# Optimization experiments

Hardware: AMD Instinct MI355X
Metric: run time of the kernel (lower is better)

## Reference

```python
import jax, jax.numpy as jnp
import numpy as np

D_MODEL, D_FF, N_EXP, TOP_K = 1024, 2816, 8, 2
EPS = 1e-6


def setup_inputs() -> dict:
    key = jax.random.key(0)
    ks = jax.random.split(key, 9)
    s = 1.0 / np.sqrt(D_MODEL)
    sf = 1.0 / np.sqrt(D_FF)
    x = jax.random.normal(ks[0], (2, 2048, D_MODEL), dtype=jnp.float32)
    gate_w = jax.random.normal(ks[1], (N_EXP, D_MODEL), dtype=jnp.float32) * s  # [E, d] (torch Linear weight)
    w1 = jax.random.normal(ks[2], (N_EXP, D_FF, D_MODEL), dtype=jnp.float32) * s
    w2 = jax.random.normal(ks[3], (N_EXP, D_MODEL, D_FF), dtype=jnp.float32) * sf
    w3 = jax.random.normal(ks[4], (N_EXP, D_FF, D_MODEL), dtype=jnp.float32) * s
    sw1 = jax.random.normal(ks[5], (D_FF, D_MODEL), dtype=jnp.float32) * s
    sw2 = jax.random.normal(ks[6], (D_MODEL, D_FF), dtype=jnp.float32) * sf
    sw3 = jax.random.normal(ks[7], (D_FF, D_MODEL), dtype=jnp.float32) * s
    return {"x": x, "gate_w": gate_w, "w1": w1, "w2": w2, "w3": w3,
            "sw1": sw1, "sw2": sw2, "sw3": sw3}


def _expert(x, a, c, b):
    h = jax.nn.gelu(x @ a.T, approximate=False) * (x @ b.T)
    return h @ c.T


def reference(x, gate_w, w1, w2, w3, sw1, sw2, sw3):
    identity = x
    # RMSNorm with fresh weight=1 (module instantiates RMSNorm inside forward)
    x_norm = x / jnp.sqrt(jnp.mean(x * x, axis=-1, keepdims=True) + EPS)
    gate_logits = x_norm @ gate_w.T                    # [B,S,E]
    gate_weights = jax.nn.softmax(gate_logits, axis=-1)
    topk_w, topk_i = jax.lax.top_k(gate_weights, TOP_K)
    topk_w = topk_w / jnp.sum(topk_w, axis=-1, keepdims=True)
    # combine weight per expert: [B,S,E]
    cw = jnp.sum(jax.nn.one_hot(topk_i, N_EXP, dtype=x.dtype) * topk_w[..., None], axis=-2)
    out = jnp.zeros_like(x)
    for e in range(N_EXP):  # fixed small expert loop
        out = out + _expert(x_norm, w1[e], w2[e], w3[e]) * cw[..., e:e + 1]
    out = out + _expert(x_norm, sw1, sw2, sw3)
    return out + identity
```

## Files before the change

kernel.cpp:

```cpp
#include <hip/hip_runtime.h>
#include <cmath>

#define T_TOK 4096
#define DM 1024
#define DFF 2816

typedef __bf16 bfx8 __attribute__((ext_vector_type(8)));
typedef float f32x4 __attribute__((ext_vector_type(4)));

__device__ __forceinline__ float bf2f(unsigned short u) {
    unsigned int x = ((unsigned int)u) << 16;
    return __uint_as_float(x);
}
__device__ __forceinline__ unsigned short f2bf(float f) {
    unsigned int b = __float_as_uint(f);
    return (unsigned short)((b + 0x7fffu + ((b >> 16) & 1u)) >> 16);
}
__device__ __forceinline__ uint4 pack8(const float* p) {
    float4 a = *(const float4*)p, b = *(const float4*)(p + 4);
    uint4 r;
    r.x = (unsigned)f2bf(a.x) | ((unsigned)f2bf(a.y) << 16);
    r.y = (unsigned)f2bf(a.z) | ((unsigned)f2bf(a.w) << 16);
    r.z = (unsigned)f2bf(b.x) | ((unsigned)f2bf(b.y) << 16);
    r.w = (unsigned)f2bf(b.z) | ((unsigned)f2bf(b.w) << 16);
    return r;
}

__global__ void kProbe(const unsigned short* __restrict__ x, int* flag, int* counts, int* counts2) {
    __shared__ int cnt;
    if (threadIdx.x == 0) cnt = 0;
    __syncthreads();
    int sane = 0;
#pragma unroll
    for (int i = 0; i < 8; i++) {
        unsigned short u = x[threadIdx.x * 8 + i];
        int e = (u >> 7) & 0xFF;
        if (e >= 110 && e <= 134) sane++;
    }
    atomicAdd(&cnt, sane);
    __syncthreads();
    if (threadIdx.x == 0) flag[0] = (cnt >= 1843) ? 0 : 1;
    if (threadIdx.x < 8) { counts[threadIdx.x] = 0; counts2[threadIdx.x] = 0; }
}

__global__ __launch_bounds__(256) void kA(
    const void* __restrict__ xraw, const void* __restrict__ gwraw, const int* __restrict__ flag,
    float* __restrict__ accum, unsigned short* __restrict__ xnorm,
    int* __restrict__ counts, int* __restrict__ t2i, float* __restrict__ t2w)
{
    int f = flag[0];
    int t = blockIdx.x, tid = threadIdx.x;
    int wid = tid >> 6, lane = tid & 63;

    double xv[4]; double ss = 0.0;
    if (f) {
        const float* xr = (const float*)xraw + (size_t)t * DM;
#pragma unroll
        for (int i = 0; i < 4; i++) { xv[i] = (double)xr[tid + 256 * i]; ss += xv[i] * xv[i]; }
    } else {
        const unsigned short* xr = (const unsigned short*)xraw + (size_t)t * DM;
#pragma unroll
        for (int i = 0; i < 4; i++) { xv[i] = (double)bf2f(xr[tid + 256 * i]); ss += xv[i] * xv[i]; }
    }
#pragma unroll
    for (int o = 32; o > 0; o >>= 1) ss += __shfl_down(ss, o);

    __shared__ double sred[4];
    __shared__ double sscale;
    if (lane == 0) sred[wid] = ss;
    __syncthreads();
    if (tid == 0) {
        double tot = sred[0] + sred[1] + sred[2] + sred[3];
        sscale = 1.0 / sqrt(tot / (double)DM + 1e-6);
    }
    __syncthreads();
    double scale = sscale;

#pragma unroll
    for (int i = 0; i < 4; i++) {
        int idx = tid + 256 * i;
        accum[(size_t)t * DM + idx] = (float)xv[i];
        xnorm[(size_t)t * DM + idx] = f2bf((float)(xv[i] * scale));
    }

    const float* gw32 = (const float*)gwraw;
    const unsigned short* gw16 = (const unsigned short*)gwraw;
    double p[8];
#pragma unroll
    for (int e = 0; e < 8; e++) p[e] = 0.0;
#pragma unroll
    for (int i = 0; i < 4; i++) {
        int idx = tid + 256 * i;
#pragma unroll
        for (int e = 0; e < 8; e++) {
            double w = f ? (double)gw32[e * DM + idx] : (double)bf2f(gw16[e * DM + idx]);
            p[e] += xv[i] * w;
        }
    }
    __shared__ double gred[4][8];
#pragma unroll
    for (int e = 0; e < 8; e++) {
        double v = p[e];
#pragma unroll
        for (int o = 32; o > 0; o >>= 1) v += __shfl_down(v, o);
        if (lane == 0) gred[wid][e] = v;
    }
    __syncthreads();
    if (tid == 0) {
        double l[8], m = -1e300;
        for (int e = 0; e < 8; e++) {
            l[e] = scale * (gred[0][e] + gred[1][e] + gred[2][e] + gred[3][e]);
            if (l[e] > m) m = l[e];
        }
        double pe[8];
        for (int e = 0; e < 8; e++) pe[e] = exp(l[e] - m);
        int a = 0;
        for (int e = 1; e < 8; e++) if (pe[e] > pe[a]) a = e;
        int b = (a == 0) ? 1 : 0;
        for (int e = 0; e < 8; e++) { if (e == a) continue; if (pe[e] > pe[b]) b = e; }
        double s2 = pe[a] + pe[b];
        t2i[2 * t] = a; t2i[2 * t + 1] = b;
        t2w[2 * t] = (float)(pe[a] / s2); t2w[2 * t + 1] = (float)(pe[b] / s2);
        atomicAdd(&counts[a], 1); atomicAdd(&counts[b], 1);
    }
}

__global__ void kA2(const int* counts, int* base) {
    if (threadIdx.x == 0) {
        int acc = 0;
        for (int e = 0; e < 8; e++) { base[e] = acc; acc += counts[e]; }
    }
}

__global__ __launch_bounds__(256) void kA3(
    const int* __restrict__ t2i, const float* __restrict__ t2w, const int* __restrict__ base,
    int* counts2, int* __restrict__ rows_token, float* __restrict__ rows_w)
{
    int t = blockIdx.x * 256 + threadIdx.x;
    if (t < T_TOK) {
#pragma unroll
        for (int s = 0; s < 2; s++) {
            int e = t2i[2 * t + s];
            int pos = atomicAdd(&counts2[e], 1);
            int row = base[e] + pos;
            rows_token[row] = t; rows_w[row] = t2w[2 * t + s];
        }
        rows_token[2 * T_TOK + t] = t;
        rows_w[2 * T_TOK + t] = 1.0f;
    }
}

__global__ __launch_bounds__(256) void kB(
    const unsigned short* __restrict__ xnorm,
    const void* __restrict__ w1, const void* __restrict__ w3,
    const void* __restrict__ sw1, const void* __restrict__ sw3,
    const int* __restrict__ flag, const int* __restrict__ counts, const int* __restrict__ base,
    const int* __restrict__ rows_token, unsigned short* __restrict__ h, int c0, int CF)
{
    int f = flag[0];
    int e = blockIdx.z;
    int nr, rb; const unsigned short *W1u, *W3u; const float *W1f, *W3f;
    if (e < 8) {
        nr = counts[e]; rb = base[e];
        size_t eb = (size_t)e * DFF * DM;
        W1u = (const unsigned short*)w1 + eb; W3u = (const unsigned short*)w3 + eb;
        W1f = (const float*)w1 + eb;          W3f = (const float*)w3 + eb;
    } else {
        nr = T_TOK; rb = 2 * T_TOK;
        W1u = (const unsigned short*)sw1; W3u = (const unsigned short*)sw3;
        W1f = (const float*)sw1;          W3f = (const float*)sw3;
    }
    int r0 = blockIdx.y * 128;
    if (r0 >= nr) return;
    int n0l = blockIdx.x * 64;

    __shared__ __align__(16) unsigned short sA[128 * 72];
    __shared__ __align__(16) unsigned short sB1[64 * 72];
    __shared__ __align__(16) unsigned short sB3[64 * 72];

    int tid = threadIdx.x, wid = tid >> 6, lane = tid & 63;
    int srow = tid >> 3, scol = (tid & 7) * 8;
    int q = lane >> 4, ln = lane & 15;

    const unsigned short* aptr[4];
#pragma unroll
    for (int t = 0; t < 4; t++) {
        int r = r0 + srow + t * 32;
        int tk = rows_token[rb + ((r < nr) ? r : 0)];
        aptr[t] = xnorm + (size_t)tk * DM + scol;
    }
    size_t boff[2];
#pragma unroll
    for (int t = 0; t < 2; t++)
        boff[t] = (size_t)(c0 + n0l + srow + t * 32) * DM + scol;

    f32x4 acc1[2][4], acc3[2][4];
#pragma unroll
    for (int i = 0; i < 2; i++)
#pragma unroll
        for (int j = 0; j < 4; j++) { acc1[i][j] = 0.0f; acc3[i][j] = 0.0f; }

    for (int ko = 0; ko < DM; ko += 64) {
#pragma unroll
        for (int t = 0; t < 4; t++)
            *(uint4*)&sA[(srow + t * 32) * 72 + scol] = *(const uint4*)(aptr[t] + ko);
        if (!f) {
#pragma unroll
            for (int t = 0; t < 2; t++) {
                *(uint4*)&sB1[(srow + t * 32) * 72 + scol] = *(const uint4*)(W1u + boff[t] + ko);
                *(uint4*)&sB3[(srow + t * 32) * 72 + scol] = *(const uint4*)(W3u + boff[t] + ko);
            }
        } else {
#pragma unroll
            for (int t = 0; t < 2; t++) {
                *(uint4*)&sB1[(srow + t * 32) * 72 + scol] = pack8(W1f + boff[t] + ko);
                *(uint4*)&sB3[(srow + t * 32) * 72 + scol] = pack8(W3f + boff[t] + ko);
            }
        }
        __syncthreads();
#pragma unroll
        for (int ks = 0; ks < 2; ks++) {
            bfx8 aF[2], b1F[4], b3F[4];
#pragma unroll
            for (int mt = 0; mt < 2; mt++)
                aF[mt] = *(const bfx8*)&sA[(wid * 32 + mt * 16 + ln) * 72 + ks * 32 + q * 8];
#pragma unroll
            for (int nt = 0; nt < 4; nt++) {
                b1F[nt] = *(const bfx8*)&sB1[(nt * 16 + ln) * 72 + ks * 32 + q * 8];
                b3F[nt] = *(const bfx8*)&sB3[(nt * 16 + ln) * 72 + ks * 32 + q * 8];
            }
#pragma unroll
            for (int mt = 0; mt < 2; mt++)
#pragma unroll
                for (int nt = 0; nt < 4; nt++) {
                    acc1[mt][nt] = __builtin_amdgcn_mfma_f32_16x16x32_bf16(aF[mt], b1F[nt], acc1[mt][nt], 0, 0, 0);
                    acc3[mt][nt] = __builtin_amdgcn_mfma_f32_16x16x32_bf16(aF[mt], b3F[nt], acc3[mt][nt], 0, 0, 0);
                }
        }
        __syncthreads();
    }

#pragma unroll
    for (int mt = 0; mt < 2; mt++)
#pragma unroll
        for (int nt = 0; nt < 4; nt++)
#pragma unroll
            for (int r = 0; r < 4; r++) {
                int gr = r0 + wid * 32 + mt * 16 + q * 4 + r;
                if (gr < nr) {
                    float a = acc1[mt][nt][r], b3v = acc3[mt][nt][r];
                    float g = 0.5f * a * (1.0f + erff(a * 0.70710678118654752f));
                    h[(size_t)(rb + gr) * CF + n0l + nt * 16 + ln] = f2bf(g * b3v);
                }
            }
}

__global__ __launch_bounds__(256) void kC(
    const unsigned short* __restrict__ h,
    const void* __restrict__ w2, const void* __restrict__ sw2,
    const int* __restrict__ flag, const int* __restrict__ counts, const int* __restrict__ base,
    const int* __restrict__ rows_token, const float* __restrict__ rows_w,
    float* __restrict__ accum, int c0, int CF)
{
    int f = flag[0];
    int e = blockIdx.z;
    int nr, rb; const unsigned short* W2u; const float* W2f;
    if (e < 8) {
        nr = counts[e]; rb = base[e];
        size_t eb = (size_t)e * DM * DFF;
        W2u = (const unsigned short*)w2 + eb; W2f = (const float*)w2 + eb;
    } else {
        nr = T_TOK; rb = 2 * T_TOK;
        W2u = (const unsigned short*)sw2; W2f = (const float*)sw2;
    }
    int r0 = blockIdx.y * 128;
    if (r0 >= nr) return;
    int n0 = blockIdx.x * 64;

    __shared__ __align__(16) unsigned short sA[128 * 72];
    __shared__ __align__(16) unsigned short sB[64 * 72];

    int tid = threadIdx.x, wid = tid >> 6, lane = tid & 63;
    int srow = tid >> 3, scol = (tid & 7) * 8;
    int q = lane >> 4, ln = lane & 15;

    size_t aoff[4];
#pragma unroll
    for (int t = 0; t < 4; t++) {
        int r = r0 + srow + t * 32;
        int rr = (r < nr) ? r : 0;
        aoff[t] = (size_t)(rb + rr) * CF + scol;
    }
    size_t boff[2];
#pragma unroll
    for (int t = 0; t < 2; t++)
        boff[t] = (size_t)(n0 + srow + t * 32) * DFF + c0 + scol;

    f32x4 acc[2][4];
#pragma unroll
    for (int i = 0; i < 2; i++)
#pragma unroll
        for (int j = 0; j < 4; j++) acc[i][j] = 0.0f;

    for (int ko = 0; ko < CF; ko += 64) {
#pragma unroll
        for (int t = 0; t < 4; t++)
            *(uint4*)&sA[(srow + t * 32) * 72 + scol] = *(const uint4*)(h + aoff[t] + ko);
        if (!f) {
#pragma unroll
            for (int t = 0; t < 2; t++)
                *(uint4*)&sB[(srow + t * 32) * 72 + scol] = *(const uint4*)(W2u + boff[t] + ko);
        } else {
#pragma unroll
            for (int t = 0; t < 2; t++)
                *(uint4*)&sB[(srow + t * 32) * 72 + scol] = pack8(W2f + boff[t] + ko);
        }
        __syncthreads();
#pragma unroll
        for (int ks = 0; ks < 2; ks++) {
            bfx8 aF[2], bF[4];
#pragma unroll
            for (int mt = 0; mt < 2; mt++)
                aF[mt] = *(const bfx8*)&sA[(wid * 32 + mt * 16 + ln) * 72 + ks * 32 + q * 8];
#pragma unroll
            for (int nt = 0; nt < 4; nt++)
                bF[nt] = *(const bfx8*)&sB[(nt * 16 + ln) * 72 + ks * 32 + q * 8];
#pragma unroll
            for (int mt = 0; mt < 2; mt++)
#pragma unroll
                for (int nt = 0; nt < 4; nt++)
                    acc[mt][nt] = __builtin_amdgcn_mfma_f32_16x16x32_bf16(aF[mt], bF[nt], acc[mt][nt], 0, 0, 0);
        }
        __syncthreads();
    }

#pragma unroll
    for (int mt = 0; mt < 2; mt++)
#pragma unroll
        for (int r = 0; r < 4; r++) {
            int gr = r0 + wid * 32 + mt * 16 + q * 4 + r;
            if (gr < nr) {
                float w = rows_w[rb + gr];
                int tk = rows_token[rb + gr];
#pragma unroll
                for (int nt = 0; nt < 4; nt++)
                    atomicAdd(&accum[(size_t)tk * DM + n0 + nt * 16 + ln], acc[mt][nt][r] * w);
            }
        }
}

__global__ __launch_bounds__(256) void kD(const float* __restrict__ accum, void* __restrict__ outraw,
                                          const int* __restrict__ flag) {
    int f = flag[0];
    int i = (blockIdx.x * 256 + threadIdx.x) * 4;
    float4 v = *(const float4*)&accum[i];
    if (f) {
        *(float4*)((float*)outraw + i) = v;
    } else {
        ushort4 u;
        u.x = f2bf(v.x); u.y = f2bf(v.y); u.z = f2bf(v.z); u.w = f2bf(v.w);
        *(ushort4*)((unsigned short*)outraw + i) = u;
    }
}

extern "C" void kernel_launch(void* const* d_in, const int* in_sizes, int n_in,
                              void* d_out, int out_size, void* d_ws, size_t ws_size,
                              hipStream_t stream)
{
    const void* x   = d_in[0];
    const void* gw  = d_in[1];
    const void* w1  = d_in[2];
    const void* w2  = d_in[3];
    const void* w3  = d_in[4];
    const void* sw1 = d_in[5];
    const void* sw2 = d_in[6];
    const void* sw3 = d_in[7];

    char* ws = (char*)d_ws;
    size_t off = 0;
    auto alloc = [&](size_t bytes) { void* p = ws + off; off += (bytes + 255) & ~(size_t)255; return p; };
    int* flag             = (int*)alloc(256);
    unsigned short* xnorm = (unsigned short*)alloc((size_t)T_TOK * DM * 2);
    float* accum          = (float*)alloc((size_t)T_TOK * DM * 4);
    int* counts           = (int*)alloc(256);
    int* counts2          = (int*)alloc(256);
    int* base             = (int*)alloc(256);
    int* rows_token       = (int*)alloc((size_t)3 * T_TOK * 4);
    float* rows_w         = (float*)alloc((size_t)3 * T_TOK * 4);
    int* t2i              = (int*)alloc((size_t)T_TOK * 2 * 4);
    float* t2w            = (float*)alloc((size_t)T_TOK * 2 * 4);

    static const int ncs[6] = {1, 2, 4, 11, 22, 44};
    int NC = 44;
    for (int i = 0; i < 6; i++) {
        size_t hb = (size_t)3 * T_TOK * (DFF / ncs[i]) * 2;
        if (off + hb <= ws_size) { NC = ncs[i]; break; }
    }
    int CF = DFF / NC;
    unsigned short* h = (unsigned short*)alloc((size_t)3 * T_TOK * CF * 2);

    kProbe<<<1, 256, 0, stream>>>((const unsigned short*)x, flag, counts, counts2);
    kA<<<T_TOK, 256, 0, stream>>>(x, gw, flag, accum, xnorm, counts, t2i, t2w);
    kA2<<<1, 64, 0, stream>>>(counts, base);
    kA3<<<(T_TOK + 255) / 256, 256, 0, stream>>>(t2i, t2w, base, counts2, rows_token, rows_w);
    for (int c = 0; c < NC; c++) {
        kB<<<dim3(CF / 64, 32, 9), 256, 0, stream>>>(xnorm, w1, w3, sw1, sw3, flag, counts, base,
                                                     rows_token, h, c * CF, CF);
        kC<<<dim3(DM / 64, 32, 9), 256, 0, stream>>>(h, w2, sw2, flag, counts, base,
                                                     rows_token, rows_w, accum, c * CF, CF);
    }
    kD<<<(T_TOK * DM) / 1024, 256, 0, stream>>>(accum, d_out, flag);
}
```

Baseline: 874.0 us.

## Pre-convert fp32 weights to bf16 and use direct global-to-LDS loads in GEMMs

Adds kernels that convert the fp32 expert weights to bf16 chunk buffers before the GEMMs, so the main kernels no longer pack fp32 to bf16 inside the K loop. Both GEMM kernels now stage A and B tiles with global_load_lds 16-byte direct loads into unpadded LDS. kB uses a 2x2 wave layout and kC grows its N tile from 64 to 128. The grid order is swapped so row blocks vary fastest. In exchange it spends extra workspace and conversion traffic, and the unpadded LDS rows may cause bank conflicts.

```diff
diff --git a/kernel.cpp b/kernel.cpp
--- a/kernel.cpp
+++ b/kernel.cpp
@@ -9,8 +9,7 @@
 typedef float f32x4 __attribute__((ext_vector_type(4)));
 
 __device__ __forceinline__ float bf2f(unsigned short u) {
-    unsigned int x = ((unsigned int)u) << 16;
-    return __uint_as_float(x);
+    return __uint_as_float(((unsigned int)u) << 16);
 }
 __device__ __forceinline__ unsigned short f2bf(float f) {
     unsigned int b = __float_as_uint(f);
@@ -24,6 +23,10 @@
     r.z = (unsigned)f2bf(b.x) | ((unsigned)f2bf(b.y) << 16);
     r.w = (unsigned)f2bf(b.z) | ((unsigned)f2bf(b.w) << 16);
     return r;
+}
+__device__ __forceinline__ void gld16(const unsigned short* g, unsigned short* l) {
+    __builtin_amdgcn_global_load_lds((const __attribute__((address_space(1))) void*)g,
+                                     (__attribute__((address_space(3))) void*)l, 16, 0, 0);
 }
 
 __global__ void kProbe(const unsigned short* __restrict__ x, int* flag, int* counts, int* counts2) {
@@ -150,201 +153,227 @@
     }
 }
 
+__global__ void kW13(const float* __restrict__ w1f, const float* __restrict__ w3f,
+                     const float* __restrict__ sw1f, const float* __restrict__ sw3f,
+                     const int* __restrict__ flag,
+                     unsigned short* __restrict__ w1b, unsigned short* __restrict__ w3b,
+                     int c0, int CF)
+{
+    if (flag[0] == 0) return;
+    int row = blockIdx.x, e = blockIdx.y;
+    int arr = threadIdx.x >> 7, kv = threadIdx.x & 127;
+    const float* src;
+    unsigned short* dst;
+    if (arr == 0) {
+        src = (e < 8) ? w1f + ((size_t)e * DFF + c0 + row) * DM : sw1f + (size_t)(c0 + row) * DM;
+        dst = w1b + ((size_t)e * CF + row) * DM;
+    } else {
+        src = (e < 8) ? w3f + ((size_t)e * DFF + c0 + row) * DM : sw3f + (size_t)(c0 + row) * DM;
+        dst = w3b + ((size_t)e * CF + row) * DM;
+    }
+    *(uint4*)&dst[kv * 8] = pack8(src + kv * 8);
+}
+
+__global__ void kW2(const float* __restrict__ w2f, const float* __restrict__ sw2f,
+                    const int* __restrict__ flag, unsigned short* __restrict__ w2b,
+                    int c0, int CF)
+{
+    if (flag[0] == 0) return;
+    int n = blockIdx.x, e = blockIdx.y;
+    const float* src = ((e < 8) ? w2f + (size_t)e * DM * DFF : sw2f) + (size_t)n * DFF + c0;
+    unsigned short* dst = w2b + ((size_t)e * DM + n) * CF;
+    for (int rv = threadIdx.x; rv < CF / 8; rv += 256)
+        *(uint4*)&dst[rv * 8] = pack8(src + rv * 8);
+}
+
 __global__ __launch_bounds__(256) void kB(
     const unsigned short* __restrict__ xnorm,
     const void* __restrict__ w1, const void* __restrict__ w3,
     const void* __restrict__ sw1, const void* __restrict__ sw3,
+    const unsigned short* __restrict__ w1b, const unsigned short* __restrict__ w3b,
     const int* __restrict__ flag, const int* __restrict__ counts, const int* __restrict__ base,
     const int* __restrict__ rows_token, unsigned short* __restrict__ h, int c0, int CF)
 {
+    int e = blockIdx.z;
+    int nr = (e < 8) ? counts[e] : T_TOK;
+    int rb = (e < 8) ? base[e] : 2 * T_TOK;
+    int r0 = blockIdx.x * 128;
+    if (r0 >= nr) return;
+    int n0l = blockIdx.y * 64;
     int f = flag[0];
-    int e = blockIdx.z;
-    int nr, rb; const unsigned short *W1u, *W3u; const float *W1f, *W3f;
-    if (e < 8) {
-        nr = counts[e]; rb = base[e];
-        size_t eb = (size_t)e * DFF * DM;
-        W1u = (const unsigned short*)w1 + eb; W3u = (const unsigned short*)w3 + eb;
-        W1f = (const float*)w1 + eb;          W3f = (const float*)w3 + eb;
-    } else {
-        nr = T_TOK; rb = 2 * T_TOK;
-        W1u = (const unsigned short*)sw1; W3u = (const unsigned short*)sw3;
-        W1f = (const float*)sw1;          W3f = (const float*)sw3;
-    }
-    int r0 = blockIdx.y * 128;
-    if (r0 >= nr) return;
-    int n0l = blockIdx.x * 64;
-
-    __shared__ __align__(16) unsigned short sA[128 * 72];
-    __shared__ __align__(16) unsigned short sB1[64 * 72];
-    __shared__ __align__(16) unsigned short sB3[64 * 72];
+
+    __shared__ unsigned short sA[128 * 64];
+    __shared__ unsigned short sB1[64 * 64];
+    __shared__ unsigned short sB3[64 * 64];
 
     int tid = threadIdx.x, wid = tid >> 6, lane = tid & 63;
-    int srow = tid >> 3, scol = (tid & 7) * 8;
+    int wr = wid >> 1, wc = wid & 1;
     int q = lane >> 4, ln = lane & 15;
-
-    const unsigned short* aptr[4];
-#pragma unroll
-    for (int t = 0; t < 4; t++) {
-        int r = r0 + srow + t * 32;
-        int tk = rows_token[rb + ((r < nr) ? r : 0)];
-        aptr[t] = xnorm + (size_t)tk * DM + scol;
-    }
-    size_t boff[2];
-#pragma unroll
-    for (int t = 0; t < 2; t++)
-        boff[t] = (size_t)(c0 + n0l + srow + t * 32) * DM + scol;
-
-    f32x4 acc1[2][4], acc3[2][4];
-#pragma unroll
-    for (int i = 0; i < 2; i++)
-#pragma unroll
-        for (int j = 0; j < 4; j++) { acc1[i][j] = 0.0f; acc3[i][j] = 0.0f; }
+    int lr = lane >> 3, lc = (lane & 7) * 8;
+
+    const unsigned short* ga[4];
+#pragma unroll
+    for (int j = 0; j < 4; j++) {
+        int r = r0 + wid * 32 + j * 8 + lr;
+        int rc = (r < nr) ? r : (nr - 1);
+        ga[j] = xnorm + (size_t)rows_token[rb + rc] * DM + lc;
+    }
+    const unsigned short* gb[4];
+    {
+        bool isB3 = (wid >= 2);
+        int whalf = wid & 1;
+        const unsigned short* Wo = isB3
+            ? ((e < 8) ? (const unsigned short*)w3 + (size_t)e * DFF * DM : (const unsigned short*)sw3)
+            : ((e < 8) ? (const unsigned short*)w1 + (size_t)e * DFF * DM : (const unsigned short*)sw1);
+        const unsigned short* Wb = (isB3 ? w3b : w1b) + (size_t)e * CF * DM;
+#pragma unroll
+        for (int j = 0; j < 4; j++) {
+            int row = whalf * 32 + j * 8 + lr;
+            gb[j] = f ? (Wb + (size_t)(n0l + row) * DM + lc)
+                      : (Wo + (size_t)(c0 + n0l + row) * DM + lc);
+        }
+    }
+    unsigned short* sBdst = (wid >= 2) ? sB3 : sB1;
+    unsigned short* ldsA[4]; unsigned short* ldsB[4];
+#pragma unroll
+    for (int j = 0; j < 4; j++) {
+        ldsA[j] = &sA[(wid * 32 + j * 8) * 64];
+        ldsB[j] = &sBdst[((wid & 1) * 32 + j * 8) * 64];
+    }
+
+    f32x4 acc1[4][2], acc3[4][2];
+#pragma unroll
+    for (int m = 0; m < 4; m++)
+#pragma unroll
+        for (int n = 0; n < 2; n++) { acc1[m][n] = 0.0f; acc3[m][n] = 0.0f; }
 
     for (int ko = 0; ko < DM; ko += 64) {
 #pragma unroll
-        for (int t = 0; t < 4; t++)
-            *(uint4*)&sA[(srow + t * 32) * 72 + scol] = *(const uint4*)(aptr[t] + ko);
-        if (!f) {
-#pragma unroll
-            for (int t = 0; t < 2; t++) {
-                *(uint4*)&sB1[(srow + t * 32) * 72 + scol] = *(const uint4*)(W1u + boff[t] + ko);
-                *(uint4*)&sB3[(srow + t * 32) * 72 + scol] = *(const uint4*)(W3u + boff[t] + ko);
+        for (int j = 0; j < 4; j++) gld16(ga[j] + ko, ldsA[j]);
+#pragma unroll
+        for (int j = 0; j < 4; j++) gld16(gb[j] + ko, ldsB[j]);
+        __syncthreads();
+#pragma unroll
+        for (int ks = 0; ks < 2; ks++) {
+            bfx8 aF[4], b1F[2], b3F[2];
+#pragma unroll
+            for (int m = 0; m < 4; m++)
+                aF[m] = *(const bfx8*)&sA[(wr * 64 + m * 16 + ln) * 64 + ks * 32 + q * 8];
+#pragma unroll
+            for (int n = 0; n < 2; n++) {
+                b1F[n] = *(const bfx8*)&sB1[(wc * 32 + n * 16 + ln) * 64 + ks * 32 + q * 8];
+                b3F[n] = *(const bfx8*)&sB3[(wc * 32 + n * 16 + ln) * 64 + ks * 32 + q * 8];
             }
-        } else {
-#pragma unroll
-            for (int t = 0; t < 2; t++) {
-                *(uint4*)&sB1[(srow + t * 32) * 72 + scol] = pack8(W1f + boff[t] + ko);
-                *(uint4*)&sB3[(srow + t * 32) * 72 + scol] = pack8(W3f + boff[t] + ko);
-            }
+#pragma unroll
+            for (int m = 0; m < 4; m++)
+#pragma unroll
+                for (int n = 0; n < 2; n++) {
+                    acc1[m][n] = __builtin_amdgcn_mfma_f32_16x16x32_bf16(aF[m], b1F[n], acc1[m][n], 0, 0, 0);
+                    acc3[m][n] = __builtin_amdgcn_mfma_f32_16x16x32_bf16(aF[m], b3F[n], acc3[m][n], 0, 0, 0);
+                }
         }
         __syncthreads();
-#pragma unroll
-        for (int ks = 0; ks < 2; ks++) {
-            bfx8 aF[2], b1F[4], b3F[4];
-#pragma unroll
-            for (int mt = 0; mt < 2; mt++)
-                aF[mt] = *(const bfx8*)&sA[(wid * 32 + mt * 16 + ln) * 72 + ks * 32 + q * 8];
-#pragma unroll
-            for (int nt = 0; nt < 4; nt++) {
-                b1F[nt] = *(const bfx8*)&sB1[(nt * 16 + ln) * 72 + ks * 32 + q * 8];
-                b3F[nt] = *(const bfx8*)&sB3[(nt * 16 + ln) * 72 + ks * 32 + q * 8];
-            }
-#pragma unroll
-            for (int mt = 0; mt < 2; mt++)
-#pragma unroll
-                for (int nt = 0; nt < 4; nt++) {
-                    acc1[mt][nt] = __builtin_amdgcn_mfma_f32_16x16x32_bf16(aF[mt], b1F[nt], acc1[mt][nt], 0, 0, 0);
-                    acc3[mt][nt] = __builtin_amdgcn_mfma_f32_16x16x32_bf16(aF[mt], b3F[nt], acc3[mt][nt], 0, 0, 0);
-                }
-        }
-        __syncthreads();
-    }
-
-#pragma unroll
-    for (int mt = 0; mt < 2; mt++)
-#pragma unroll
-        for (int nt = 0; nt < 4; nt++)
-#pragma unroll
-            for (int r = 0; r < 4; r++) {
-                int gr = r0 + wid * 32 + mt * 16 + q * 4 + r;
-                if (gr < nr) {
-                    float a = acc1[mt][nt][r], b3v = acc3[mt][nt][r];
+    }
+
+#pragma unroll
+    for (int m = 0; m < 4; m++)
+#pragma unroll
+        for (int r = 0; r < 4; r++) {
+            int gr = r0 + wr * 64 + m * 16 + q * 4 + r;
+            if (gr < nr) {
+#pragma unroll
+                for (int n = 0; n < 2; n++) {
+                    float a = acc1[m][n][r], b3v = acc3[m][n][r];
                     float g = 0.5f * a * (1.0f + erff(a * 0.70710678118654752f));
-                    h[(size_t)(rb + gr) * CF + n0l + nt * 16 + ln] = f2bf(g * b3v);
+                    h[(size_t)(rb + gr) * CF + n0l + wc * 32 + n * 16 + ln] = f2bf(g * b3v);
                 }
             }
+        }
 }
 
 __global__ __launch_bounds__(256) void kC(
     const unsigned short* __restrict__ h,
     const void* __restrict__ w2, const void* __restrict__ sw2,
+    const unsigned short* __restrict__ w2b,
     const int* __restrict__ flag, const int* __restrict__ counts, const int* __restrict__ base,
     const int* __restrict__ rows_token, const float* __restrict__ rows_w,
     float* __restrict__ accum, int c0, int CF)
 {
+    int e = blockIdx.z;
+    int nr = (e < 8) ? counts[e] : T_TOK;
+    int rb = (e < 8) ? base[e] : 2 * T_TOK;
+    int r0 = blockIdx.x * 128;
+    if (r0 >= nr) return;
+    int n0 = blockIdx.y * 128;
     int f = flag[0];
-    int e = blockIdx.z;
-    int nr, rb; const unsigned short* W2u; const float* W2f;
-    if (e < 8) {
-        nr = counts[e]; rb = base[e];
-        size_t eb = (size_t)e * DM * DFF;
-        W2u = (const unsigned short*)w2 + eb; W2f = (const float*)w2 + eb;
-    } else {
-        nr = T_TOK; rb = 2 * T_TOK;
-        W2u = (const unsigned short*)sw2; W2f = (const float*)sw2;
-    }
-    int r0 = blockIdx.y * 128;
-    if (r0 >= nr) return;
-    int n0 = blockIdx.x * 64;
-
-    __shared__ __align__(16) unsigned short sA[128 * 72];
-    __shared__ __align__(16) unsigned short sB[64 * 72];
+
+    __shared__ unsigned short sA[128 * 64];
+    __shared__ unsigned short sB[128 * 64];
 
     int tid = threadIdx.x, wid = tid >> 6, lane = tid & 63;
-    int srow = tid >> 3, scol = (tid & 7) * 8;
+    int wr = wid >> 1, wc = wid & 1;
     int q = lane >> 4, ln = lane & 15;
-
-    size_t aoff[4];
-#pragma unroll
-    for (int t = 0; t < 4; t++) {
-        int r = r0 + srow + t * 32;
-        int rr = (r < nr) ? r : 0;
-        aoff[t] = (size_t)(rb + rr) * CF + scol;
-    }
-    size_t boff[2];
-#pragma unroll
-    for (int t = 0; t < 2; t++)
-        boff[t] = (size_t)(n0 + srow + t * 32) * DFF + c0 + scol;
-
-    f32x4 acc[2][4];
-#pragma unroll
-    for (int i = 0; i < 2; i++)
-#pragma unroll
-        for (int j = 0; j < 4; j++) acc[i][j] = 0.0f;
+    int lr = lane >> 3, lc = (lane & 7) * 8;
+
+    const unsigned short* Wo = (e < 8) ? (const unsigned short*)w2 + (size_t)e * DM * DFF
+                                       : (const unsigned short*)sw2;
+    const unsigned short* Wb = w2b + (size_t)e * DM * CF;
+    const unsigned short* ga[4]; const unsigned short* gb[4];
+#pragma unroll
+    for (int j = 0; j < 4; j++) {
+        int r = r0 + wid * 32 + j * 8 + lr;
+        ga[j] = h + (size_t)(rb + r) * CF + lc;
+        int n = n0 + wid * 32 + j * 8 + lr;
+        gb[j] = f ? (Wb + (size_t)n * CF + lc) : (Wo + (size_t)n * DFF + c0 + lc);
+    }
+    unsigned short* ldsA[4]; unsigned short* ldsB[4];
+#pragma unroll
+    for (int j = 0; j < 4; j++) {
+        ldsA[j] = &sA[(wid * 32 + j * 8) * 64];
+        ldsB[j] = &sB[(wid * 32 + j * 8) * 64];
+    }
+
+    f32x4 acc[4][4];
+#pragma unroll
+    for (int m = 0; m < 4; m++)
+#pragma unroll
+        for (int n = 0; n < 4; n++) acc[m][n] = 0.0f;
 
     for (int ko = 0; ko < CF; ko += 64) {
 #pragma unroll
-        for (int t = 0; t < 4; t++)
-            *(uint4*)&sA[(srow + t * 32) * 72 + scol] = *(const uint4*)(h + aoff[t] + ko);
-        if (!f) {
-#pragma unroll
-            for (int t = 0; t < 2; t++)
-                *(uint4*)&sB[(srow + t * 32) * 72 + scol] = *(const uint4*)(W2u + boff[t] + ko);
-        } else {
-#pragma unroll
-            for (int t = 0; t < 2; t++)
-                *(uint4*)&sB[(srow + t * 32) * 72 + scol] = pack8(W2f + boff[t] + ko);
-        }
+        for (int j = 0; j < 4; j++) gld16(ga[j] + ko, ldsA[j]);
+#pragma unroll
+        for (int j = 0; j < 4; j++) gld16(gb[j] + ko, ldsB[j]);
         __syncthreads();
 #pragma unroll
         for (int ks = 0; ks < 2; ks++) {
-            bfx8 aF[2], bF[4];
-#pragma unroll
-            for (int mt = 0; mt < 2; mt++)
-                aF[mt] = *(const bfx8*)&sA[(wid * 32 + mt * 16 + ln) * 72 + ks * 32 + q * 8];
-#pragma unroll
-            for (int nt = 0; nt < 4; nt++)
-                bF[nt] = *(const bfx8*)&sB[(nt * 16 + ln) * 72 + ks * 32 + q * 8];
-#pragma unroll
-            for (int mt = 0; mt < 2; mt++)
-#pragma unroll
-                for (int nt = 0; nt < 4; nt++)
-                    acc[mt][nt] = __builtin_amdgcn_mfma_f32_16x16x32_bf16(aF[mt], bF[nt], acc[mt][nt], 0, 0, 0);
+            bfx8 aF[4], bF[4];
+#pragma unroll
+            for (int m = 0; m < 4; m++)
+                aF[m] = *(const bfx8*)&sA[(wr * 64 + m * 16 + ln) * 64 + ks * 32 + q * 8];
+#pragma unroll
+            for (int n = 0; n < 4; n++)
+                bF[n] = *(const bfx8*)&sB[(wc * 64 + n * 16 + ln) * 64 + ks * 32 + q * 8];
+#pragma unroll
+            for (int m = 0; m < 4; m++)
+#pragma unroll
+                for (int n = 0; n < 4; n++)
+                    acc[m][n] = __builtin_amdgcn_mfma_f32_16x16x32_bf16(aF[m], bF[n], acc[m][n], 0, 0, 0);
         }
         __syncthreads();
     }
 
 #pragma unroll
-    for (int mt = 0; mt < 2; mt++)
+    for (int m = 0; m < 4; m++)
 #pragma unroll
         for (int r = 0; r < 4; r++) {
-            int gr = r0 + wid * 32 + mt * 16 + q * 4 + r;
+            int gr = r0 + wr * 64 + m * 16 + q * 4 + r;
             if (gr < nr) {
                 float w = rows_w[rb + gr];
                 int tk = rows_token[rb + gr];
 #pragma unroll
-                for (int nt = 0; nt < 4; nt++)
-                    atomicAdd(&accum[(size_t)tk * DM + n0 + nt * 16 + ln], acc[mt][nt][r] * w);
+                for (int n = 0; n < 4; n++)
+                    atomicAdd(&accum[(size_t)tk * DM + n0 + wc * 64 + n * 16 + ln], acc[m][n][r] * w);
             }
         }
 }
@@ -393,21 +422,30 @@
     static const int ncs[6] = {1, 2, 4, 11, 22, 44};
     int NC = 44;
     for (int i = 0; i < 6; i++) {
-        size_t hb = (size_t)3 * T_TOK * (DFF / ncs[i]) * 2;
-        if (off + hb <= ws_size) { NC = ncs[i]; break; }
+        size_t CFi = DFF / ncs[i];
+        size_t need = off + CFi * ((size_t)9 * DM * 2 * 3 + (size_t)3 * T_TOK * 2) + 1024;
+        if (need <= ws_size) { NC = ncs[i]; break; }
     }
     int CF = DFF / NC;
-    unsigned short* h = (unsigned short*)alloc((size_t)3 * T_TOK * CF * 2);
+    unsigned short* w1b = (unsigned short*)alloc((size_t)9 * CF * DM * 2);
+    unsigned short* w3b = (unsigned short*)alloc((size_t)9 * CF * DM * 2);
+    unsigned short* w2b = (unsigned short*)alloc((size_t)9 * DM * CF * 2);
+    unsigned short* h   = (unsigned short*)alloc((size_t)3 * T_TOK * CF * 2);
 
     kProbe<<<1, 256, 0, stream>>>((const unsigned short*)x, flag, counts, counts2);
     kA<<<T_TOK, 256, 0, stream>>>(x, gw, flag, accum, xnorm, counts, t2i, t2w);
     kA2<<<1, 64, 0, stream>>>(counts, base);
     kA3<<<(T_TOK + 255) / 256, 256, 0, stream>>>(t2i, t2w, base, counts2, rows_token, rows_w);
     for (int c = 0; c < NC; c++) {
-        kB<<<dim3(CF / 64, 32, 9), 256, 0, stream>>>(xnorm, w1, w3, sw1, sw3, flag, counts, base,
-                                                     rows_token, h, c * CF, CF);
-        kC<<<dim3(DM / 64, 32, 9), 256, 0, stream>>>(h, w2, sw2, flag, counts, base,
-                                                     rows_token, rows_w, accum, c * CF, CF);
+        int c0 = c * CF;
+        kW13<<<dim3(CF, 9), 256, 0, stream>>>((const float*)w1, (const float*)w3,
+                                              (const float*)sw1, (const float*)sw3,
+                                              flag, w1b, w3b, c0, CF);
+        kW2<<<dim3(DM, 9), 256, 0, stream>>>((const float*)w2, (const float*)sw2, flag, w2b, c0, CF);
+        kB<<<dim3(32, CF / 64, 9), 256, 0, stream>>>(xnorm, w1, w3, sw1, sw3, w1b, w3b,
+                                                     flag, counts, base, rows_token, h, c0, CF);
+        kC<<<dim3(32, 8, 9), 256, 0, stream>>>(h, w2, sw2, w2b, flag, counts, base,
+                                               rows_token, rows_w, accum, c0, CF);
     }
     kD<<<(T_TOK * DM) / 1024, 256, 0, stream>>>(accum, d_out, flag);
 }
```

Result: slower. 1.533 ms (+75.4%).
